# Optimization experiments

Measured on AMD Instinct MI355X. Metric: run time of the kernel, lower is better.

The kernel has to match this reference:

```python
import jax, jax.numpy as jnp
import numpy as np

N, D, H, DATT, C, NCLS = 20000, 1024, 512, 256, 10, 4

def setup_inputs() -> dict:
    key = jax.random.key(0)
    ks = jax.random.split(key, 20)
    s = lambda fan_in: 1.0 / np.sqrt(fan_in)
    u = lambda k, shape, fan_in: jax.random.uniform(k, shape, jnp.float32, -s(fan_in), s(fan_in))
    inp = {
        'x': jax.random.normal(ks[0], (N, D), jnp.float32),
        'cluster_id': jax.random.randint(ks[1], (N,), 0, C),
        # per-cluster expert MLP (phi_i): Linear(D,H)+ReLU, Linear(H,H)+ReLU (dropout=identity in eval)
        'W1': u(ks[2], (C, D, H), D), 'b1': u(ks[3], (C, H), D),
        'W2': u(ks[4], (C, H, H), H), 'b2': u(ks[5], (C, H), H),
        # attention_net: Linear(H,H)+ReLU then gated attention (L=H, D=DATT, n_classes=1)
        'fc_W': u(ks[6], (H, H), H), 'fc_b': u(ks[7], (H,), H),
        'Wa': u(ks[8], (H, DATT), H), 'ba': u(ks[9], (DATT,), H),
        'Wb': u(ks[10], (H, DATT), H), 'bb': u(ks[11], (DATT,), H),
        'Wc': u(ks[12], (DATT, 1), DATT), 'bc': u(ks[13], (1,), DATT),
        # rho: Linear(H, DATT)+ReLU
        'rho_W': u(ks[14], (H, DATT), H), 'rho_b': u(ks[15], (DATT,), H),
        # classifier
        'cls_W': u(ks[16], (DATT, NCLS), DATT), 'cls_b': u(ks[17], (NCLS,), DATT),
    }
    return inp

def reference(x, cluster_id, W1, b1, W2, b2, fc_W, fc_b, Wa, ba, Wb, bb, Wc, bc, rho_W, rho_b, cls_W, cls_b):
    # --- per-cluster expert MLPs, vectorized over clusters (no python loop over data) ---
    # h1: [C, N, H] = ReLU(x @ W1_c + b1_c) for every cluster c
    h1 = jax.nn.relu(jnp.einsum('nd,cdh->cnh', x, W1) + b1[:, None, :])
    h2 = jax.nn.relu(jnp.einsum('cnh,chk->cnk', h1, W2) + b2[:, None, :])
    # masked mean-pool per cluster (AdaptiveAvgPool1d(1) over the cluster's tokens)
    mask = (cluster_id[None, :] == jnp.arange(C)[:, None]).astype(h2.dtype)  # [C, N]
    counts = jnp.maximum(mask.sum(axis=1), 1.0)                               # empty cluster -> zeros
    h_cluster = jnp.einsum('cn,cnh->ch', mask, h2) / counts[:, None]          # [C, H]
    # --- attention net: fc + gated attention ---
    h = jax.nn.relu(h_cluster @ fc_W + fc_b)                                  # [C, H]
    a = jnp.tanh(h @ Wa + ba)
    b = jax.nn.sigmoid(h @ Wb + bb)
    A = ((a * b) @ Wc + bc).T                                                 # [1, C]
    A = jax.nn.softmax(A, axis=1)
    h_path = A @ h                                                            # [1, H]
    hr = jax.nn.relu(h_path @ rho_W + rho_b)[0]                               # [DATT] (squeeze)
    logits = (hr @ cls_W + cls_b)[None, :]                                    # [1, NCLS]
    Y_prob = jax.nn.softmax(logits, axis=1)
    Y_hat = jnp.argmax(logits, axis=1, keepdims=True)
    return (logits, Y_prob, Y_hat)
```

## Files before the change

kernel.cpp:

```cpp
#include <hip/hip_runtime.h>
#include <hip/hip_bf16.h>
#include <stdint.h>

#define NT 20000
#define DIM 1024
#define HID 512
#define DATT_N 256
#define NCLUS 10
#define NCLS_N 4
#define NBS 79
#define NRT2 313

typedef __bf16 bf16;
typedef __attribute__((ext_vector_type(8))) __bf16 bf16x8;
typedef __attribute__((ext_vector_type(4))) float f32x4;

__device__ __forceinline__ void gload_lds16(const void* g, void* l) {
  __builtin_amdgcn_global_load_lds(
      (const __attribute__((address_space(1))) unsigned int*)g,
      (__attribute__((address_space(3))) unsigned int*)l, 16, 0, 0);
}


#define ZPB 20
#define TW1B (32 * 4 * NCLUS)
#define TW2B (16 * 4 * NCLUS)

__device__ __forceinline__ void tr_body(const float* __restrict__ s, bf16* __restrict__ d,
                                        int R, int Cc, int i0, int j0, float (*t)[128]) {
  int tid = threadIdx.x;
  int cr = tid >> 5;
  int cc4 = (tid & 31) << 2;
#pragma unroll
  for (int yy = 0; yy < 32; yy += 8)
    *(f32x4*)&t[yy + cr][cc4] = *(const f32x4*)&s[(size_t)(i0 + yy + cr) * Cc + j0 + cc4];
  __syncthreads();
  int col = tid >> 1, h = (tid & 1) << 4;
  bf16 tmp[16];
#pragma unroll
  for (int k = 0; k < 16; ++k) tmp[k] = (bf16)t[h + k][col];
  *(bf16x8*)&d[(size_t)(j0 + col) * R + i0 + h] = *(bf16x8*)&tmp[0];
  *(bf16x8*)&d[(size_t)(j0 + col) * R + i0 + h + 8] = *(bf16x8*)&tmp[8];
}

__global__ __launch_bounds__(256) void setup_kernel(
    const int* __restrict__ cid, int* __restrict__ blkcnt, float* __restrict__ pool,
    const float* __restrict__ W1, bf16* __restrict__ w1t,
    const float* __restrict__ W2, bf16* __restrict__ w2t) {
  __shared__ float t[32][128];
  __shared__ int wcnt[4][16];
  int b = blockIdx.x;
  int tid = threadIdx.x;
  if (b < NBS) {
    int lane = tid & 63, w = tid >> 6;
    int n = b * 256 + tid;
    int mycid = (n < NT) ? cid[n] : -1;
#pragma unroll
    for (int c = 0; c < NCLUS; ++c) {
      unsigned long long m = __ballot(mycid == c);
      if (lane == c) wcnt[w][c] = __popcll(m);
    }
    __syncthreads();
    if (tid < NCLUS)
      blkcnt[b * NCLUS + tid] =
          wcnt[0][tid] + wcnt[1][tid] + wcnt[2][tid] + wcnt[3][tid];
  } else if (b < NBS + ZPB) {
    int i = (b - NBS) * 256 + tid;
    if (i < NCLUS * HID) pool[i] = 0.f;
  } else if (b < NBS + ZPB + TW1B) {
    int bb = b - NBS - ZPB;
    int z = bb >> 7, r = bb & 127, rt = r >> 2, ct = r & 3;
    tr_body(W1 + (size_t)z * DIM * HID, w1t + (size_t)z * DIM * HID,
            DIM, HID, rt * 32, ct * 128, t);
  } else {
    int bb = b - NBS - ZPB - TW1B;
    int z = bb >> 6, r = bb & 63, rt = r >> 2, ct = r & 3;
    tr_body(W2 + (size_t)z * HID * HID, w2t + (size_t)z * HID * HID,
            HID, HID, rt * 32, ct * 128, t);
  }
}


__global__ __launch_bounds__(256) void scatter_kernel(
    const int* __restrict__ cid, const int* __restrict__ blkcnt,
    int* __restrict__ cnt, int* __restrict__ offs, int* __restrict__ order) {
  __shared__ int sbase[16];
  __shared__ int scnt[16];
  __shared__ int soffs[16];
  __shared__ int wcnt[4][16];
  __shared__ int wbase[4][16];
  int tid = threadIdx.x;
  int lane = tid & 63, w = tid >> 6;
  int bx = blockIdx.x;
  if (tid < NCLUS) {
    int base = 0, run = 0;
    for (int b = 0; b < NBS; ++b) {
      int v = blkcnt[b * NCLUS + tid];
      if (b < bx) base += v;
      run += v;
    }
    sbase[tid] = base;
    scnt[tid] = run;
  }
  __syncthreads();
  if (tid == 0) {
    int a = 0;
    for (int i = 0; i < NCLUS; ++i) { soffs[i] = a; a += scnt[i]; }
    soffs[NCLUS] = a;
  }
  __syncthreads();
  if (bx == 0 && tid <= NCLUS) {
    if (tid < NCLUS) cnt[tid] = scnt[tid];
    offs[tid] = soffs[tid];
  }
  int n = bx * 256 + tid;
  int mycid = (n < NT) ? cid[n] : -1;
  unsigned long long lmask = (lane == 63) ? ~0ull >> 1 : (1ull << lane) - 1;
  int myrank = 0;
#pragma unroll
  for (int c = 0; c < NCLUS; ++c) {
    unsigned long long m = __ballot(mycid == c);
    if (mycid == c) myrank = __popcll(m & lmask);
    if (lane == c) wcnt[w][c] = __popcll(m);
  }
  __syncthreads();
  if (tid < NCLUS) {
    int pre = sbase[tid];
#pragma unroll
    for (int ww = 0; ww < 4; ++ww) { wbase[ww][tid] = pre; pre += wcnt[ww][tid]; }
  }
  __syncthreads();
  if (n < NT) order[soffs[mycid] + wbase[w][mycid] + myrank] = n;
}

__device__ __forceinline__ bool decode_grp2(int d, int& c, int& rt, int& j) {
  int x8 = d & 7, s = d >> 3;
  int g = (s >> 2) * 8 + x8;
  if (g >= NRT2 * NCLUS) return false;
  j = s & 3;
  c = g / NRT2;
  rt = g - c * NRT2;
  return true;
}


__global__ __launch_bounds__(128, 2) void gemm1_kernel(
    const float* __restrict__ x, const int* __restrict__ order,
    const bf16* __restrict__ w1t, const float* __restrict__ b1,
    const int* __restrict__ offs, const int* __restrict__ cnt, bf16* __restrict__ h1) {
  int c, rt, j;
  if (!decode_grp2(blockIdx.x, c, rt, j)) return;
  int cntc = cnt[c];
  int row0 = rt * 64;
  if (row0 >= cntc) return;
  int seg = offs[c];
  int n0 = j * 128;

  __shared__ float Af[64 * 64];
  __shared__ bf16 Bls[128 * 64];
  __shared__ int s_ord[64];

  int tid = threadIdx.x;
  int lane = tid & 63, w = tid >> 6;
  if (tid < 64) {
    int ar = seg + row0 + tid; if (ar > NT - 1) ar = NT - 1;
    s_ord[tid] = order[ar];
  }
  __syncthreads();

  int rx = lane & 7, hi = lane >> 4;
  int kswz = ((lane & 7) ^ (lane >> 3)) << 3;

  const bf16* bptr[8]; int boff[8];
#pragma unroll
  for (int i = 0; i < 8; ++i) {
    int ch = i * 2 + w;
    int r = ch * 8 + (lane >> 3);
    bptr[i] = w1t + (size_t)(c * HID + n0 + r) * DIM + kswz;
    boff[i] = ch * 512;
  }
  const float* fptr[8]; int foff[8];
#pragma unroll
  for (int i = 0; i < 8; ++i) {
    int ch = i * 2 + w;
    int r = ch * 4 + (lane >> 4);
    int j16 = lane & 15;
    int colf = ((((j16 >> 1) ^ (r & 7)) << 1) | (j16 & 1)) << 2;
    fptr[i] = x + (size_t)s_ord[r] * DIM + colf;
    foff[i] = ch * 256;
  }

  f32x4 acc[2][8];
#pragma unroll
  for (int m = 0; m < 2; m++)
#pragma unroll
    for (int n = 0; n < 8; n++) acc[m][n] = {0.f, 0.f, 0.f, 0.f};

  for (int k0 = 0; k0 < DIM; k0 += 64) {
#pragma unroll
    for (int i = 0; i < 8; ++i) gload_lds16(fptr[i] + k0, &Af[foff[i]]);
#pragma unroll
    for (int i = 0; i < 8; ++i) gload_lds16(bptr[i] + k0, &Bls[boff[i]]);
    __syncthreads();
#pragma unroll
    for (int ks = 0; ks < 2; ++ks) {
      int pp = ks * 4 + hi;
      int kof = ((pp ^ rx) << 3);
      int kob = ((pp ^ rx) << 3);
      bf16x8 a[2], b[8];
#pragma unroll
      for (int m = 0; m < 2; m++) {
        int rr = w * 32 + m * 16 + (lane & 15);
        const f32x4* ap = (const f32x4*)&Af[rr * 64 + kof];
        f32x4 u = ap[0], v = ap[1];
        bf16x8 t;
        t[0] = (bf16)u[0]; t[1] = (bf16)u[1]; t[2] = (bf16)u[2]; t[3] = (bf16)u[3];
        t[4] = (bf16)v[0]; t[5] = (bf16)v[1]; t[6] = (bf16)v[2]; t[7] = (bf16)v[3];
        a[m] = t;
      }
#pragma unroll
      for (int n = 0; n < 8; n++)
        b[n] = *(const bf16x8*)(&Bls[(n * 16 + (lane & 15)) * 64 + kob]);
#pragma unroll
      for (int m = 0; m < 2; m++)
#pragma unroll
        for (int n = 0; n < 8; n++)
          acc[m][n] = __builtin_amdgcn_mfma_f32_16x16x32_bf16(a[m], b[n], acc[m][n], 0, 0, 0);
    }
    __syncthreads();
  }

  int valid = cntc - row0; if (valid > 64) valid = 64;
#pragma unroll
  for (int n = 0; n < 8; n++) {
    int col = n0 + n * 16 + (lane & 15);
    float bias = b1[c * HID + col];
#pragma unroll
    for (int m = 0; m < 2; m++) {
      int rbase = w * 32 + m * 16 + ((lane >> 4) << 2);
#pragma unroll
      for (int e = 0; e < 4; e++) {
        int r = rbase + e;
        if (r < valid) {
          float v = acc[m][n][e] + bias;
          h1[(size_t)(seg + row0 + r) * HID + col] = (bf16)(v > 0.f ? v : 0.f);
        }
      }
    }
  }
}


__global__ __launch_bounds__(128, 3) void gemm2_kernel(
    const bf16* __restrict__ h1, const bf16* __restrict__ w2t, const float* __restrict__ b2,
    const int* __restrict__ offs, const int* __restrict__ cnt, float* __restrict__ pool) {
  int c, rt, j;
  if (!decode_grp2(blockIdx.x, c, rt, j)) return;
  int cntc = cnt[c];
  int row0 = rt * 64;
  if (row0 >= cntc) return;
  int seg = offs[c];
  int n0 = j * 128;
  int valid = cntc - row0; if (valid > 64) valid = 64;

  __shared__ bf16 Als[64 * 64];
  __shared__ bf16 Bls[128 * 64];

  int tid = threadIdx.x;
  int lane = tid & 63, w = tid >> 6;
  int rx = lane & 7, hi = lane >> 4;
  int kswz = ((lane & 7) ^ (lane >> 3)) << 3;

  const bf16* aptr[4]; int aoff[4];
  const bf16* bptr[8]; int boff[8];
#pragma unroll
  for (int i = 0; i < 4; ++i) {
    int ch = i * 2 + w;
    int r = ch * 8 + (lane >> 3);
    int ar = seg + row0 + r; if (ar > NT - 1) ar = NT - 1;
    aptr[i] = h1 + (size_t)ar * HID + kswz;
    aoff[i] = ch * 512;
  }
#pragma unroll
  for (int i = 0; i < 8; ++i) {
    int ch = i * 2 + w;
    int r = ch * 8 + (lane >> 3);
    bptr[i] = w2t + (size_t)(c * HID + n0 + r) * HID + kswz;
    boff[i] = ch * 512;
  }

  f32x4 acc[2][8];
#pragma unroll
  for (int m = 0; m < 2; m++)
#pragma unroll
    for (int n = 0; n < 8; n++) acc[m][n] = {0.f, 0.f, 0.f, 0.f};

  for (int k0 = 0; k0 < HID; k0 += 64) {
#pragma unroll
    for (int i = 0; i < 4; ++i) gload_lds16(aptr[i] + k0, &Als[aoff[i]]);
#pragma unroll
    for (int i = 0; i < 8; ++i) gload_lds16(bptr[i] + k0, &Bls[boff[i]]);
    __syncthreads();
#pragma unroll
    for (int ks = 0; ks < 2; ++ks) {
      int t16 = ks * 4 + hi;
      int ko = ((t16 ^ rx) << 3);
      bf16x8 a[2], b[8];
#pragma unroll
      for (int m = 0; m < 2; m++)
        a[m] = *(const bf16x8*)(&Als[(w * 32 + m * 16 + (lane & 15)) * 64 + ko]);
#pragma unroll
      for (int n = 0; n < 8; n++)
        b[n] = *(const bf16x8*)(&Bls[(n * 16 + (lane & 15)) * 64 + ko]);
#pragma unroll
      for (int m = 0; m < 2; m++)
#pragma unroll
        for (int n = 0; n < 8; n++)
          acc[m][n] = __builtin_amdgcn_mfma_f32_16x16x32_bf16(a[m], b[n], acc[m][n], 0, 0, 0);
    }
    __syncthreads();
  }

#pragma unroll
  for (int n = 0; n < 8; n++) {
    int col = n0 + n * 16 + (lane & 15);
    float bias = b2[c * HID + col];
    float s = 0.f;
#pragma unroll
    for (int m = 0; m < 2; m++) {
      int rbase = w * 32 + m * 16 + ((lane >> 4) << 2);
#pragma unroll
      for (int e = 0; e < 4; e++) {
        if (rbase + e < valid) {
          float v = acc[m][n][e] + bias;
          s += (v > 0.f ? v : 0.f);
        }
      }
    }
    s += __shfl_xor(s, 16);
    s += __shfl_xor(s, 32);
    if (lane < 16) atomicAdd(&pool[c * HID + col], s);
  }
}


__global__ __launch_bounds__(256) void tail_fc(
    const float* __restrict__ pool, const int* __restrict__ cnt,
    const float* __restrict__ fcW, const float* __restrict__ fcb,
    float* __restrict__ hbuf) {
  int c = blockIdx.x >> 3;
  int jt = blockIdx.x & 7;
  __shared__ float hc[HID];
  __shared__ float red[4][64];
  int tid = threadIdx.x;
  float inv = 1.f / fmaxf((float)cnt[c], 1.f);
  for (int k = tid; k < HID; k += 256) hc[k] = pool[c * HID + k] * inv;
  __syncthreads();
  int jl = tid & 63, kg = tid >> 6;
  int j = jt * 64 + jl;
  float s = 0.f;
#pragma unroll 4
  for (int k = kg * 128; k < kg * 128 + 128; ++k) s += hc[k] * fcW[(size_t)k * HID + j];
  red[kg][jl] = s;
  __syncthreads();
  if (kg == 0) {
    float v = red[0][jl] + red[1][jl] + red[2][jl] + red[3][jl] + fcb[j];
    hbuf[c * HID + j] = fmaxf(v, 0.f);
  }
}

__global__ __launch_bounds__(1024) void tail_att(
    const float* __restrict__ hbuf,
    const float* __restrict__ Wa, const float* __restrict__ ba,
    const float* __restrict__ Wb, const float* __restrict__ bb,
    const float* __restrict__ Wc, const float* __restrict__ bc,
    float* __restrict__ score) {
  int c = blockIdx.x;
  __shared__ float h[HID];
  __shared__ float ra[4][DATT_N];
  __shared__ float rb[4][DATT_N];
  __shared__ float sc[DATT_N];
  int tid = threadIdx.x;
  for (int k = tid; k < HID; k += 1024) h[k] = hbuf[c * HID + k];
  __syncthreads();
  int jl = tid & 255, kg = tid >> 8;
  float sa = 0.f, sb = 0.f;
#pragma unroll 4
  for (int k = kg * 128; k < kg * 128 + 128; ++k) {
    float hv = h[k];
    sa += hv * Wa[(size_t)k * DATT_N + jl];
    sb += hv * Wb[(size_t)k * DATT_N + jl];
  }
  ra[kg][jl] = sa;
  rb[kg][jl] = sb;
  __syncthreads();
  if (kg == 0) {
    float va = ra[0][jl] + ra[1][jl] + ra[2][jl] + ra[3][jl] + ba[jl];
    float vb = rb[0][jl] + rb[1][jl] + rb[2][jl] + rb[3][jl] + bb[jl];
    float av = tanhf(va);
    float bv = 1.f / (1.f + expf(-vb));
    sc[jl] = av * bv * Wc[jl];
  }
  __syncthreads();
  for (int s2 = 128; s2 > 0; s2 >>= 1) {
    if (tid < s2) sc[tid] += sc[tid + s2];
    __syncthreads();
  }
  if (tid == 0) score[c] = sc[0] + bc[0];
}

__global__ __launch_bounds__(1024) void tail_fin(
    const float* __restrict__ score, const float* __restrict__ hbuf,
    const float* __restrict__ rhoW, const float* __restrict__ rhob,
    const float* __restrict__ clsW, const float* __restrict__ clsb,
    float* __restrict__ out) {
  __shared__ float Asm[NCLUS];
  __shared__ float hp[HID];
  __shared__ float rr[4][DATT_N];
  __shared__ float hr[DATT_N];
  __shared__ float lg[NCLS_N];
  int tid = threadIdx.x;
  if (tid == 0) {
    float mx = -1e30f;
    for (int c = 0; c < NCLUS; c++) mx = fmaxf(mx, score[c]);
    float sum = 0.f, e[NCLUS];
    for (int c = 0; c < NCLUS; c++) { e[c] = expf(score[c] - mx); sum += e[c]; }
    for (int c = 0; c < NCLUS; c++) Asm[c] = e[c] / sum;
  }
  __syncthreads();
  if (tid < HID) {
    float s = 0.f;
#pragma unroll
    for (int c = 0; c < NCLUS; c++) s += Asm[c] * hbuf[c * HID + tid];
    hp[tid] = s;
  }
  __syncthreads();
  int jl = tid & 255, kg = tid >> 8;
  float s = 0.f;
#pragma unroll 4
  for (int k = kg * 128; k < kg * 128 + 128; ++k) s += hp[k] * rhoW[(size_t)k * DATT_N + jl];
  rr[kg][jl] = s;
  __syncthreads();
  if (kg == 0) hr[jl] = fmaxf(rr[0][jl] + rr[1][jl] + rr[2][jl] + rr[3][jl] + rhob[jl], 0.f);
  __syncthreads();
  if (tid < NCLS_N * 64) {
    int t = tid >> 6, l = tid & 63;
    float cs = 0.f;
    for (int j = l; j < DATT_N; j += 64) cs += hr[j] * clsW[j * NCLS_N + t];
#pragma unroll
    for (int w = 32; w > 0; w >>= 1) cs += __shfl_xor(cs, w);
    if (l == 0) lg[t] = cs + clsb[t];
  }
  __syncthreads();
  if (tid == 0) {
    float mx = lg[0];
    int am = 0;
    for (int t = 1; t < NCLS_N; t++) if (lg[t] > mx) { mx = lg[t]; am = t; }
    float sum = 0.f, e[NCLS_N];
    for (int t = 0; t < NCLS_N; t++) { e[t] = expf(lg[t] - mx); sum += e[t]; }
    for (int t = 0; t < NCLS_N; t++) {
      out[t] = lg[t];
      out[NCLS_N + t] = e[t] / sum;
    }
    out[2 * NCLS_N] = (float)am;
  }
}


extern "C" void kernel_launch(void* const* d_in, const int* in_sizes, int n_in,
                              void* d_out, int out_size, void* d_ws, size_t ws_size,
                              hipStream_t stream) {
  const float* x    = (const float*)d_in[0];
  const int*   cid  = (const int*)d_in[1];
  const float* W1   = (const float*)d_in[2];
  const float* b1   = (const float*)d_in[3];
  const float* W2   = (const float*)d_in[4];
  const float* b2   = (const float*)d_in[5];
  const float* fcW  = (const float*)d_in[6];
  const float* fcb  = (const float*)d_in[7];
  const float* Wa   = (const float*)d_in[8];
  const float* ba   = (const float*)d_in[9];
  const float* Wb   = (const float*)d_in[10];
  const float* bb   = (const float*)d_in[11];
  const float* Wc   = (const float*)d_in[12];
  const float* bc   = (const float*)d_in[13];
  const float* rhoW = (const float*)d_in[14];
  const float* rhob = (const float*)d_in[15];
  const float* clsW = (const float*)d_in[16];
  const float* clsb = (const float*)d_in[17];
  float* out = (float*)d_out;

  char* ws = (char*)d_ws;
  int*   cnt     = (int*)(ws + 0);
  int*   offs    = (int*)(ws + 64);
  float* score   = (float*)(ws + 128);
  int*   blkcnt  = (int*)(ws + 256);
  int*   order   = (int*)(ws + 256 + 4096);
  float* pool    = (float*)(ws + 256 + 4096 + 80000);
  float* hbuf    = (float*)(ws + 256 + 4096 + 80000 + NCLUS * HID * 4);
  size_t o = 256 + 4096 + 80000 + 2ull * NCLUS * HID * 4;
  o = (o + 255) & ~(size_t)255;
  bf16* w1t = (bf16*)(ws + o); o += (size_t)NCLUS * HID * DIM * 2;
  bf16* w2t = (bf16*)(ws + o); o += (size_t)NCLUS * HID * HID * 2;
  bf16* h1  = (bf16*)(ws + o); o += (size_t)NT * HID * 2;

  setup_kernel<<<dim3(NBS + ZPB + TW1B + TW2B), dim3(256), 0, stream>>>(
      cid, blkcnt, pool, W1, w1t, W2, w2t);
  scatter_kernel<<<dim3(NBS), dim3(256), 0, stream>>>(cid, blkcnt, cnt, offs, order);

  int nblk = 8 * ((NRT2 * NCLUS + 7) / 8) * 4;
  gemm1_kernel<<<dim3(nblk), dim3(128), 0, stream>>>(x, order, w1t, b1, offs, cnt, h1);
  gemm2_kernel<<<dim3(nblk), dim3(128), 0, stream>>>(h1, w2t, b2, offs, cnt, pool);

  tail_fc<<<dim3(NCLUS * 8), dim3(256), 0, stream>>>(pool, cnt, fcW, fcb, hbuf);
  tail_att<<<dim3(NCLUS), dim3(1024), 0, stream>>>(hbuf, Wa, ba, Wb, bb, Wc, bc, score);
  tail_fin<<<dim3(1), dim3(1024), 0, stream>>>(score, hbuf, rhoW, rhob, clsW, clsb, out);
}
```

Measured before the change: 137.5 us.

## Double-buffer W1 tiles and stage x through registers as bf16 in gemm1

The gemm1 main loop now double-buffers the W1 tile in LDS, issuing the next tile's async global-to-LDS loads before computing on the current one. Instead of loading fp32 x tiles into LDS and converting them on every fragment read, each thread prefetches its x slice into registers one iteration ahead, converts it once to bf16, and writes it to a swizzled bf16 LDS buffer. The goal is to overlap global memory latency with MFMA work and cut A-tile LDS traffic and conversion work. The cost is more registers (prefetched x plus all A and B fragments held at once) and handwritten barrier and waitcnt sequencing, which could limit occupancy or introduce a race on the buffers.

```diff
diff --git a/kernel.cpp b/kernel.cpp
--- a/kernel.cpp
+++ b/kernel.cpp
@@ -156,8 +156,8 @@
   int seg = offs[c];
   int n0 = j * 128;
 
-  __shared__ float Af[64 * 64];
-  __shared__ bf16 Bls[128 * 64];
+  __shared__ bf16 Als[64 * 64];
+  __shared__ bf16 Bls[2][128 * 64];
   __shared__ int s_ord[64];
 
   int tid = threadIdx.x;
@@ -179,16 +179,8 @@
     bptr[i] = w1t + (size_t)(c * HID + n0 + r) * DIM + kswz;
     boff[i] = ch * 512;
   }
-  const float* fptr[8]; int foff[8];
-#pragma unroll
-  for (int i = 0; i < 8; ++i) {
-    int ch = i * 2 + w;
-    int r = ch * 4 + (lane >> 4);
-    int j16 = lane & 15;
-    int colf = ((((j16 >> 1) ^ (r & 7)) << 1) | (j16 & 1)) << 2;
-    fptr[i] = x + (size_t)s_ord[r] * DIM + colf;
-    foff[i] = ch * 256;
-  }
+  int arow = tid >> 1, ah = tid & 1;
+  const float* fa = x + (size_t)s_ord[arow] * DIM + ah * 32;
 
   f32x4 acc[2][8];
 #pragma unroll
@@ -196,38 +188,60 @@
 #pragma unroll
     for (int n = 0; n < 8; n++) acc[m][n] = {0.f, 0.f, 0.f, 0.f};
 
-  for (int k0 = 0; k0 < DIM; k0 += 64) {
-#pragma unroll
-    for (int i = 0; i < 8; ++i) gload_lds16(fptr[i] + k0, &Af[foff[i]]);
-#pragma unroll
-    for (int i = 0; i < 8; ++i) gload_lds16(bptr[i] + k0, &Bls[boff[i]]);
-    __syncthreads();
+#pragma unroll
+  for (int i = 0; i < 8; ++i) gload_lds16(bptr[i], &Bls[0][boff[i]]);
+  f32x4 areg[8];
+#pragma unroll
+  for (int i = 0; i < 8; ++i) areg[i] = *(const f32x4*)(fa + i * 4);
+
+  const int NKT = DIM / 64;
+#pragma unroll 2
+  for (int t = 0; t < NKT; ++t) {
+    if (t + 1 < NKT) {
+#pragma unroll
+      for (int i = 0; i < 8; ++i)
+        gload_lds16(bptr[i] + (t + 1) * 64, &Bls[(t + 1) & 1][boff[i]]);
+    }
+#pragma unroll
+    for (int i = 0; i < 4; ++i) {
+      f32x4 u = areg[2 * i], v = areg[2 * i + 1];
+      bf16x8 tb;
+      tb[0] = (bf16)u[0]; tb[1] = (bf16)u[1]; tb[2] = (bf16)u[2]; tb[3] = (bf16)u[3];
+      tb[4] = (bf16)v[0]; tb[5] = (bf16)v[1]; tb[6] = (bf16)v[2]; tb[7] = (bf16)v[3];
+      int s = ah * 4 + i;
+      *(bf16x8*)&Als[arow * 64 + (((s ^ (arow & 7)) << 3))] = tb;
+    }
+    asm volatile("s_waitcnt lgkmcnt(0)" ::: "memory");
+    __builtin_amdgcn_s_barrier();
+    asm volatile("" ::: "memory");
+
+    bf16x8 a[2][2], b[2][8];
+    const bf16* Bb = &Bls[t & 1][0];
 #pragma unroll
     for (int ks = 0; ks < 2; ++ks) {
-      int pp = ks * 4 + hi;
-      int kof = ((pp ^ rx) << 3);
-      int kob = ((pp ^ rx) << 3);
-      bf16x8 a[2], b[8];
-#pragma unroll
-      for (int m = 0; m < 2; m++) {
-        int rr = w * 32 + m * 16 + (lane & 15);
-        const f32x4* ap = (const f32x4*)&Af[rr * 64 + kof];
-        f32x4 u = ap[0], v = ap[1];
-        bf16x8 t;
-        t[0] = (bf16)u[0]; t[1] = (bf16)u[1]; t[2] = (bf16)u[2]; t[3] = (bf16)u[3];
-        t[4] = (bf16)v[0]; t[5] = (bf16)v[1]; t[6] = (bf16)v[2]; t[7] = (bf16)v[3];
-        a[m] = t;
-      }
+      int t16 = ks * 4 + hi;
+      int ko = ((t16 ^ rx) << 3);
+#pragma unroll
+      for (int m = 0; m < 2; m++)
+        a[ks][m] = *(const bf16x8*)(&Als[(w * 32 + m * 16 + (lane & 15)) * 64 + ko]);
 #pragma unroll
       for (int n = 0; n < 8; n++)
-        b[n] = *(const bf16x8*)(&Bls[(n * 16 + (lane & 15)) * 64 + kob]);
+        b[ks][n] = *(const bf16x8*)(&Bb[(n * 16 + (lane & 15)) * 64 + ko]);
+    }
+    if (t + 1 < NKT) {
+#pragma unroll
+      for (int i = 0; i < 8; ++i) areg[i] = *(const f32x4*)(fa + (t + 1) * 64 + i * 4);
+    }
+#pragma unroll
+    for (int ks = 0; ks < 2; ++ks)
 #pragma unroll
       for (int m = 0; m < 2; m++)
 #pragma unroll
         for (int n = 0; n < 8; n++)
-          acc[m][n] = __builtin_amdgcn_mfma_f32_16x16x32_bf16(a[m], b[n], acc[m][n], 0, 0, 0);
-    }
-    __syncthreads();
+          acc[m][n] = __builtin_amdgcn_mfma_f32_16x16x32_bf16(a[ks][m], b[ks][n], acc[m][n], 0, 0, 0);
+    asm volatile("" ::: "memory");
+    __builtin_amdgcn_s_barrier();
+    asm volatile("" ::: "memory");
   }
 
   int valid = cntc - row0; if (valid > 64) valid = 64;
```

After: 161.0 us. 1.17x slower.
